# Performance work log

Measured on AMD Instinct MI355X. Metric: run time of the kernel, lower is better.

The kernel has to match this reference:

```python
import jax, jax.numpy as jnp
import numpy as np
import math

K = 3          # kernel_size
P_GEM = 3.0    # GeM power
EPS_GEM = 1e-6
EPS_NORM = 1e-12


def _l2n(x, axis):
    n = jnp.sqrt(jnp.sum(x * x, axis=axis, keepdims=True))
    return x / jnp.maximum(n, EPS_NORM)


def setup_inputs() -> dict:
    key = jax.random.key(0)
    ks = jax.random.split(key, 7)
    b, hw, c, nc = 32, 196, 768, 4096
    hidden = c  # mlp_ratio = 1
    return {
        "patch_tokens": jax.random.normal(ks[0], (b, hw, c), dtype=jnp.float32),
        "fc1_w": jax.random.normal(ks[1], (c, hidden), dtype=jnp.float32) * 0.02,
        "fc1_b": jnp.zeros((hidden,), dtype=jnp.float32),
        "fc2_w": jax.random.normal(ks[2], (hidden, c), dtype=jnp.float32) * 0.02,
        "fc2_b": jnp.zeros((c,), dtype=jnp.float32),
        "head_w": jax.random.normal(ks[3], (c, nc), dtype=jnp.float32) * 0.02,
        "head_b": jnp.zeros((nc,), dtype=jnp.float32),
    }


def reference(patch_tokens, fc1_w, fc1_b, fc2_w, fc2_b, head_w, head_b):
    b, hw, c = patch_tokens.shape
    h = w = int(math.sqrt(hw))

    # ---- SpaceSelfAware: pad -> unfold (3x3 local windows) -> multiply ----
    img = jnp.transpose(patch_tokens, (0, 2, 1)).reshape(b, c, h, w)
    # ZeroPad2d((left=1, right=1, top=2, bottom=0)) for kernel_size=3
    padded = jnp.pad(img, ((0, 0), (0, 0), (K - 1, 0), (K // 2, K // 2)))
    # stack the 9 shifted views, row-major over (ki, kj) matching nn.Unfold
    wins = jnp.stack(
        [padded[:, :, ki:ki + h, kj:kj + w] for ki in range(K) for kj in range(K)],
        axis=2,
    )  # (b, c, 9, h, w)
    y = wins.reshape(b, c, K, K, hw)
    y = jnp.transpose(y, (0, 4, 1, 2, 3))  # (b, hw, c, K, K)
    ssa = patch_tokens[:, :, :, None, None] * y  # (b, hw, c, K, K)

    # ---- space_fusion: L2Norm(dim=1) then GeM(p=3) over the KxK window ----
    ssa = _l2n(ssa, axis=1)
    pooled = jnp.mean(jnp.clip(ssa, EPS_GEM, None) ** P_GEM, axis=(-2, -1)) ** (1.0 / P_GEM)  # (b, hw, c)

    # ---- residual + L2 normalize over channels + Mlp ----
    tokens = pooled + patch_tokens
    tokens = _l2n(tokens, axis=-1)
    hdn = jax.nn.gelu(tokens @ fc1_w + fc1_b, approximate=False)
    tokens = hdn @ fc2_w + fc2_b  # (b, hw, c)

    # ---- GeMHead: GeM(p=3) over tokens, linear to nc, L2 normalize ----
    g = jnp.mean(jnp.clip(tokens, EPS_GEM, None) ** P_GEM, axis=1) ** (1.0 / P_GEM)  # (b, c)
    desc = g @ head_w + head_b  # (b, nc)
    desc = _l2n(desc, axis=-1)
    return desc
```

## Files before the change

### kernel.cpp

```cpp
#include <hip/hip_runtime.h>
#include <hip/hip_bf16.h>
#include <math.h>

#define B   32
#define P   196
#define C   768
#define NC  4096
#define HH  14
#define KSPLIT 24
#define NT  12
#define M6  6272
#define TW  (768 * 32)
#define TM  (M6 * 32)

typedef _Float16 half8 __attribute__((ext_vector_type(8)));
typedef _Float16 half4 __attribute__((ext_vector_type(4)));
typedef float f32x4 __attribute__((ext_vector_type(4)));

#define GLOAD_LDS16(g, l)                                                      \
    __builtin_amdgcn_global_load_lds(                                          \
        (const __attribute__((address_space(1))) void*)(g),                    \
        (__attribute__((address_space(3))) void*)(l), 16, 0, 0)

__global__ __launch_bounds__(256) void k_ssa(const float* __restrict__ t,
                                             float* __restrict__ pre) {
    const int b = blockIdx.y, c0 = blockIdx.x * 16;
    __shared__ float xp_[256 * 16];
    __shared__ float part[4][9][16];
    __shared__ float inv_norm[9][16];
    const int tid = threadIdx.x;
    const int cc = tid & 15, g = tid >> 4, wv = tid >> 6;

#pragma unroll
    for (int q = 0; q < 16; ++q) xp_[q * 256 + tid] = 0.0f;
    __syncthreads();

    for (int idx = tid; idx < 784; idx += 256) {
        const int p = idx >> 2, c = (idx & 3) * 4;
        const int i = p / HH, j = p % HH;
        *(float4*)&xp_[((i + 2) * 16 + (j + 1)) * 16 + c] =
            *(const float4*)&t[((size_t)b * P + p) * C + c0 + c];
    }
    __syncthreads();

    float s[9] = {};
    {
        int i = 0, j = g;
        if (j >= HH) { j -= HH; i = 1; }
        for (int p = g; p < P; p += 16) {
            const int base = ((i + 2) * 16 + (j + 1)) * 16 + cc;
            const float xp = xp_[base];
            const float xp2 = xp * xp;
#pragma unroll
            for (int k = 0; k < 9; ++k) {
                const int off = ((k / 3) - 2) * 16 + (k % 3) - 1;
                const float nb = xp_[base + off * 16];
                s[k] += xp2 * nb * nb;
            }
            j += 2; ++i;
            if (j >= HH) { j -= HH; ++i; }
        }
    }
#pragma unroll
    for (int k = 0; k < 9; ++k) {
        float r = s[k];
        r += __shfl_xor(r, 16);
        r += __shfl_xor(r, 32);
        s[k] = r;
    }
    if ((tid & 63) < 16) {
#pragma unroll
        for (int k = 0; k < 9; ++k) part[wv][k][cc] = s[k];
    }
    __syncthreads();
    if (tid < 144) {
        const int k = tid >> 4, c2 = tid & 15;
        const float t4 = part[0][k][c2] + part[1][k][c2] +
                         part[2][k][c2] + part[3][k][c2];
        inv_norm[k][c2] = 1.0f / fmaxf(sqrtf(t4), 1e-12f);
    }
    __syncthreads();

    float invn[9];
#pragma unroll
    for (int k = 0; k < 9; ++k) invn[k] = inv_norm[k][cc];

    {
        int i = 0, j = g;
        if (j >= HH) { j -= HH; i = 1; }
        for (int p = g; p < P; p += 16) {
            const int base = ((i + 2) * 16 + (j + 1)) * 16 + cc;
            const float xp = xp_[base];
            float acc = 0.0f;
#pragma unroll
            for (int k = 0; k < 9; ++k) {
                const int off = ((k / 3) - 2) * 16 + (k % 3) - 1;
                const float v = xp * xp_[base + off * 16];
                const float u = fmaxf(v * invn[k], 1e-6f);
                acc += u * u * u;
            }
            pre[((size_t)b * P + p) * C + c0 + cc] =
                cbrtf(acc * (1.0f / 9.0f)) + xp;
            j += 2; ++i;
            if (j >= HH) { j -= HH; ++i; }
        }
    }
}

__global__ __launch_bounds__(256) void k_rownorm(const float* __restrict__ in,
                                                 _Float16* __restrict__ outP) {
    const int row = blockIdx.x;
    const float* r = in + (size_t)row * C;
    const int tid = threadIdx.x;
    float vals[3];
    float s = 0.0f;
#pragma unroll
    for (int q = 0; q < 3; ++q) {
        vals[q] = r[tid + q * 256];
        s += vals[q] * vals[q];
    }
    __shared__ float partial[4];
    __shared__ float inv;
    __shared__ _Float16 nrm[C];
#pragma unroll
    for (int off = 32; off > 0; off >>= 1) s += __shfl_xor(s, off);
    if ((tid & 63) == 0) partial[tid >> 6] = s;
    __syncthreads();
    if (tid == 0)
        inv = 1.0f / fmaxf(sqrtf(partial[0] + partial[1] + partial[2] + partial[3]), 1e-12f);
    __syncthreads();
#pragma unroll
    for (int q = 0; q < 3; ++q)
        nrm[tid + q * 256] = (_Float16)(vals[q] * inv);
    __syncthreads();
    if (tid < 96) {
        const half8 v = *(const half8*)&nrm[tid * 8];
        const int kb = tid >> 2;
        const int slot = (tid & 3) ^ ((row >> 1) & 3);
        *(half8*)&outP[(size_t)kb * TM + (size_t)row * 32 + slot * 8] = v;
    }
}

__global__ __launch_bounds__(256) void k_wt(const float* __restrict__ W,
                                            _Float16* __restrict__ WtP) {
    __shared__ float tt[32][33];
    const int k0 = blockIdx.x * 32, n0 = blockIdx.y * 32;
    const int r = threadIdx.x / 32, c = threadIdx.x % 32;
#pragma unroll
    for (int q = 0; q < 4; ++q)
        tt[r + q * 8][c] = W[(size_t)(k0 + r + q * 8) * C + n0 + c];
    __syncthreads();
    const int nl = threadIdx.x >> 3, h = threadIdx.x & 7;
    const int n = n0 + nl;
    half4 v;
#pragma unroll
    for (int j = 0; j < 4; ++j) v[j] = (_Float16)tt[h * 4 + j][nl];
    const int el = (h * 4) ^ (((n >> 1) & 3) << 3);
    *(half4*)&WtP[(size_t)blockIdx.x * TW + (size_t)n * 32 + el] = v;
}

template <bool GELU>
__global__ __launch_bounds__(256) void k_mfma_gemm(
    const _Float16* __restrict__ TokP,
    const _Float16* __restrict__ WtP,
    const float* __restrict__ bias,
    _Float16* __restrict__ Cout) {
    __shared__ _Float16 lA[3][2][64][32];
    __shared__ _Float16 lB[3][2][64][32];
    const int tid = threadIdx.x;
    const int w = tid >> 6, l = tid & 63;
    const int l15 = l & 15, lk = l >> 4;

    const int lid = blockIdx.x;
    int vm, vn;
    if (lid < 1152) { vm = (lid / 96) * 8 + (lid & 7); vn = (lid % 96) >> 3; }
    else            { const int r = lid - 1152; vm = 96 + r / 12; vn = r % 12; }
    const int m0 = vm * 64, n0 = vn * 64;
    const int wn = (w & 1) * 32, wm = (w >> 1) * 32;

    f32x4 acc[2][2] = {};

    const int kbsel = w & 1;
    const bool isB = (w >= 2);
    const _Float16* srcBase =
        isB ? (TokP + (size_t)m0 * 32) : (WtP + (size_t)n0 * 32);
    const size_t tileStride = isB ? (size_t)TM : (size_t)TW;
    _Float16* dst0 = isB ? &lB[0][kbsel][0][0] : &lA[0][kbsel][0][0];

#define ISSUE(tt, bf_)                                                         \
    {   const _Float16* s_ = srcBase + (size_t)(2 * (tt) + kbsel) * tileStride;\
        _Float16* d_ = dst0 + (size_t)(bf_) * 4096;                            \
        GLOAD_LDS16(s_ + l * 8,        d_ + l * 8);                            \
        GLOAD_LDS16(s_ + 512 + l * 8,  d_ + 512 + l * 8);                      \
        GLOAD_LDS16(s_ + 1024 + l * 8, d_ + 1024 + l * 8);                     \
        GLOAD_LDS16(s_ + 1536 + l * 8, d_ + 1536 + l * 8); }

    ISSUE(0, 0); ISSUE(1, 1); ISSUE(2, 2);

    for (int t = 0; t < NT; ++t) {
        if (t < NT - 2)       asm volatile("s_waitcnt vmcnt(8)" ::: "memory");
        else if (t == NT - 2) asm volatile("s_waitcnt vmcnt(4)" ::: "memory");
        else                  asm volatile("s_waitcnt vmcnt(0)" ::: "memory");
        __builtin_amdgcn_s_barrier();
        __builtin_amdgcn_sched_barrier(0);

        const int buf = t % 3;
#pragma unroll
        for (int kk = 0; kk < 2; ++kk) {
            half8 af[2], bf[2];
#pragma unroll
            for (int fa = 0; fa < 2; ++fa) {
                const int rowA = wn + fa * 16 + l15;
                const int colA = (lk ^ ((rowA >> 1) & 3)) * 8;
                af[fa] = *(const half8*)&lA[buf][kk][rowA][colA];
            }
#pragma unroll
            for (int fb = 0; fb < 2; ++fb) {
                const int rowB = wm + fb * 16 + l15;
                const int colB = (lk ^ ((rowB >> 1) & 3)) * 8;
                bf[fb] = *(const half8*)&lB[buf][kk][rowB][colB];
            }
#pragma unroll
            for (int fa = 0; fa < 2; ++fa)
#pragma unroll
                for (int fb = 0; fb < 2; ++fb)
                    acc[fa][fb] = __builtin_amdgcn_mfma_f32_16x16x32_f16(
                        af[fa], bf[fb], acc[fa][fb], 0, 0, 0);
        }
        asm volatile("s_waitcnt lgkmcnt(0)" ::: "memory");
        __builtin_amdgcn_s_barrier();
        __builtin_amdgcn_sched_barrier(0);
        if (t < NT - 3) ISSUE(t + 3, buf);
    }
#undef ISSUE

#pragma unroll
    for (int fa = 0; fa < 2; ++fa) {
        const int nb = n0 + wn + fa * 16 + lk * 4;
        const float4 bv = *(const float4*)&bias[nb];
#pragma unroll
        for (int fb = 0; fb < 2; ++fb) {
            const int m = m0 + wm + fb * 16 + l15;
            half4 o;
            if (GELU) {
#pragma unroll
                for (int rr = 0; rr < 4; ++rr) {
                    float v = acc[fa][fb][rr] + ((const float*)&bv)[rr];
                    v = 0.5f * v * (1.0f + erff(v * 0.70710678118654752f));
                    o[rr] = (_Float16)v;
                }
                const int el = (nb & 31) ^ (((m >> 1) & 3) << 3);
                *(half4*)&Cout[(size_t)(nb >> 5) * TM + (size_t)m * 32 + el] = o;
            } else {
#pragma unroll
                for (int rr = 0; rr < 4; ++rr)
                    o[rr] = (_Float16)(acc[fa][fb][rr] + ((const float*)&bv)[rr]);
                *(half4*)&Cout[(size_t)m * C + nb] = o;
            }
        }
    }
}

__global__ __launch_bounds__(256) void k_gempool(const _Float16* __restrict__ tk,
                                                 float* __restrict__ g) {
    const int b = blockIdx.x / 12;
    const int c0 = (blockIdx.x % 12) * 64;
    const int tid = threadIdx.x;
    const int cc = tid & 63, pg = tid >> 6;
    float s = 0.0f;
    for (int p = pg * 49; p < pg * 49 + 49; ++p) {
        const float v = fmaxf((float)tk[((size_t)b * P + p) * C + c0 + cc], 1e-6f);
        s += v * v * v;
    }
    __shared__ float part[4][64];
    part[pg][cc] = s;
    __syncthreads();
    if (tid < 64) {
        const float t4 = part[0][cc] + part[1][cc] + part[2][cc] + part[3][cc];
        g[b * C + c0 + cc] = cbrtf(t4 * (1.0f / (float)P));
    }
}

__global__ __launch_bounds__(256) void k_head1(const float* __restrict__ g,
                                               const float* __restrict__ W,
                                               float* __restrict__ partial) {
    const int n0 = blockIdx.x * 64;
    const int k0 = blockIdx.y * 32;
    __shared__ float gs[32][32];
    __shared__ float part[4][32][64];
    const int tid = threadIdx.x;

    for (int idx = tid; idx < 32 * 32; idx += 256)
        gs[idx >> 5][idx & 31] = g[(idx >> 5) * C + k0 + (idx & 31)];
    __syncthreads();

    const int c = tid & 63, q = tid >> 6;
    float acc[32] = {};
#pragma unroll
    for (int kk = 0; kk < 8; ++kk) {
        const int k = q * 8 + kk;
        const float wv = W[(size_t)(k0 + k) * NC + n0 + c];
#pragma unroll
        for (int b = 0; b < 32; ++b) acc[b] += gs[b][k] * wv;
    }
#pragma unroll
    for (int b = 0; b < 32; ++b) part[q][b][c] = acc[b];
    __syncthreads();

    for (int o = tid; o < 32 * 64; o += 256) {
        const int b = o >> 6, cc = o & 63;
        const float v = part[0][b][cc] + part[1][b][cc] +
                        part[2][b][cc] + part[3][b][cc];
        partial[((size_t)blockIdx.y * 32 + b) * NC + n0 + cc] = v;
    }
}

__global__ __launch_bounds__(256) void k_head2(const float* __restrict__ partial,
                                               const float* __restrict__ hb,
                                               float* __restrict__ out) {
    const int n = blockIdx.x * 256 + threadIdx.x;
    const int b = blockIdx.y;
    float s = hb[n];
#pragma unroll
    for (int ks = 0; ks < KSPLIT; ++ks)
        s += partial[((size_t)ks * 32 + b) * NC + n];
    out[(size_t)b * NC + n] = s;
}

__global__ __launch_bounds__(256) void k_outnorm(float* __restrict__ out) {
    const int b = blockIdx.x;
    float* r = out + (size_t)b * NC;
    const int tid = threadIdx.x;
    float v[16];
    float s = 0.0f;
#pragma unroll
    for (int q = 0; q < 16; ++q) {
        v[q] = r[tid + q * 256];
        s += v[q] * v[q];
    }
    __shared__ float partial[4];
    __shared__ float inv;
#pragma unroll
    for (int off = 32; off > 0; off >>= 1) s += __shfl_xor(s, off);
    if ((tid & 63) == 0) partial[tid >> 6] = s;
    __syncthreads();
    if (tid == 0)
        inv = 1.0f / fmaxf(sqrtf(partial[0] + partial[1] + partial[2] + partial[3]), 1e-12f);
    __syncthreads();
#pragma unroll
    for (int q = 0; q < 16; ++q) r[tid + q * 256] = v[q] * inv;
}

extern "C" void kernel_launch(void* const* d_in, const int* in_sizes, int n_in,
                              void* d_out, int out_size, void* d_ws, size_t ws_size,
                              hipStream_t stream) {
    const float* patch  = (const float*)d_in[0];
    const float* fc1_w  = (const float*)d_in[1];
    const float* fc1_b  = (const float*)d_in[2];
    const float* fc2_w  = (const float*)d_in[3];
    const float* fc2_b  = (const float*)d_in[4];
    const float* head_w = (const float*)d_in[5];
    const float* head_b = (const float*)d_in[6];
    float* out = (float*)d_out;

    const size_t big = (size_t)B * P * C;
    float*    pre  = (float*)d_ws;
    _Float16* tokP = (_Float16*)(pre + big);
    _Float16* hdnP = tokP + big;
    _Float16* wt1  = hdnP + big;
    _Float16* wt2  = wt1 + C * C;
    float*    gbuf = (float*)(wt2 + C * C);
    float*    hpart = gbuf + B * C;
    _Float16* tok2 = (_Float16*)pre;

    k_ssa<<<dim3(C / 16, B), dim3(256), 0, stream>>>(patch, pre);
    k_wt<<<dim3(C / 32, C / 32), dim3(256), 0, stream>>>(fc1_w, wt1);
    k_wt<<<dim3(C / 32, C / 32), dim3(256), 0, stream>>>(fc2_w, wt2);
    k_rownorm<<<dim3(B * P), dim3(256), 0, stream>>>(pre, tokP);
    k_mfma_gemm<true><<<dim3(1176), dim3(256), 0, stream>>>(
        tokP, wt1, fc1_b, hdnP);
    k_mfma_gemm<false><<<dim3(1176), dim3(256), 0, stream>>>(
        hdnP, wt2, fc2_b, tok2);
    k_gempool<<<dim3(B * 12), dim3(256), 0, stream>>>(tok2, gbuf);
    k_head1<<<dim3(NC / 64, KSPLIT), dim3(256), 0, stream>>>(gbuf, head_w, hpart);
    k_head2<<<dim3(NC / 256, B), dim3(256), 0, stream>>>(hpart, head_b, out);
    k_outnorm<<<dim3(B), dim3(256), 0, stream>>>(out);
}
```

Baseline: 94.03 us.

## Fold row normalization into fc1 epilogue and emit packed fp16 from SSA

The SSA kernel now writes unnormalized fp16 tokens directly in the swizzled GEMM layout, together with per-channel-block partial sums of squares. A small kernel reduces these partials into per-row inverse norms, and the fc1 GEMM epilogue multiplies the accumulator by that inverse norm. This removes the fp32 intermediate write/read and the separate row-norm kernel, and the two weight transposes are merged into one launch. The trade-off is that fp16 rounding now happens before normalization rather than after, and there is an extra partial-sum buffer and reduction kernel.

```diff
diff --git a/kernel.cpp b/kernel.cpp
--- a/kernel.cpp
+++ b/kernel.cpp
@@ -23,11 +23,13 @@
         (__attribute__((address_space(3))) void*)(l), 16, 0, 0)
 
 __global__ __launch_bounds__(256) void k_ssa(const float* __restrict__ t,
-                                             float* __restrict__ pre) {
-    const int b = blockIdx.y, c0 = blockIdx.x * 16;
+                                             _Float16* __restrict__ outP,
+                                             float* __restrict__ partial) {
+    const int b = blockIdx.y, cb = blockIdx.x, c0 = cb * 16;
     __shared__ float xp_[256 * 16];
     __shared__ float part[4][9][16];
     __shared__ float inv_norm[9][16];
+    __shared__ _Float16 outT[P][16];
     const int tid = threadIdx.x;
     const int cc = tid & 15, g = tid >> 4, wv = tid >> 6;
 
@@ -99,50 +101,46 @@
                 const float u = fmaxf(v * invn[k], 1e-6f);
                 acc += u * u * u;
             }
-            pre[((size_t)b * P + p) * C + c0 + cc] =
-                cbrtf(acc * (1.0f / 9.0f)) + xp;
+            const float val = cbrtf(acc * (1.0f / 9.0f)) + xp;
+            float rs = val * val;
+            rs += __shfl_xor(rs, 1);
+            rs += __shfl_xor(rs, 2);
+            rs += __shfl_xor(rs, 4);
+            rs += __shfl_xor(rs, 8);
+            outT[p][cc] = (_Float16)val;
+            if (cc == 0) partial[(size_t)cb * M6 + b * P + p] = rs;
             j += 2; ++i;
             if (j >= HH) { j -= HH; ++i; }
         }
     }
-}
-
-__global__ __launch_bounds__(256) void k_rownorm(const float* __restrict__ in,
-                                                 _Float16* __restrict__ outP) {
-    const int row = blockIdx.x;
-    const float* r = in + (size_t)row * C;
-    const int tid = threadIdx.x;
-    float vals[3];
-    float s = 0.0f;
-#pragma unroll
-    for (int q = 0; q < 3; ++q) {
-        vals[q] = r[tid + q * 256];
-        s += vals[q] * vals[q];
-    }
-    __shared__ float partial[4];
-    __shared__ float inv;
-    __shared__ _Float16 nrm[C];
-#pragma unroll
-    for (int off = 32; off > 0; off >>= 1) s += __shfl_xor(s, off);
-    if ((tid & 63) == 0) partial[tid >> 6] = s;
-    __syncthreads();
-    if (tid == 0)
-        inv = 1.0f / fmaxf(sqrtf(partial[0] + partial[1] + partial[2] + partial[3]), 1e-12f);
-    __syncthreads();
-#pragma unroll
-    for (int q = 0; q < 3; ++q)
-        nrm[tid + q * 256] = (_Float16)(vals[q] * inv);
-    __syncthreads();
-    if (tid < 96) {
-        const half8 v = *(const half8*)&nrm[tid * 8];
-        const int kb = tid >> 2;
-        const int slot = (tid & 3) ^ ((row >> 1) & 3);
+    __syncthreads();
+    const int kb = cb >> 1, kbase = (cb & 1) * 16;
+    for (int idx = tid; idx < P * 2; idx += 256) {
+        const int p = idx >> 1, h = idx & 1;
+        const half8 v = *(const half8*)&outT[p][h * 8];
+        const int row = b * P + p;
+        const int slot = ((kbase + h * 8) >> 3) ^ ((row >> 1) & 3);
         *(half8*)&outP[(size_t)kb * TM + (size_t)row * 32 + slot * 8] = v;
     }
 }
 
-__global__ __launch_bounds__(256) void k_wt(const float* __restrict__ W,
-                                            _Float16* __restrict__ WtP) {
+__global__ __launch_bounds__(256) void k_inv(const float* __restrict__ partial,
+                                             float* __restrict__ inv) {
+    const int row = blockIdx.x * 256 + threadIdx.x;
+    if (row < M6) {
+        float s = 0.0f;
+#pragma unroll 8
+        for (int cb = 0; cb < 48; ++cb) s += partial[(size_t)cb * M6 + row];
+        inv[row] = 1.0f / fmaxf(sqrtf(s), 1e-12f);
+    }
+}
+
+__global__ __launch_bounds__(256) void k_wt(const float* __restrict__ W1,
+                                            const float* __restrict__ W2,
+                                            _Float16* __restrict__ O1,
+                                            _Float16* __restrict__ O2) {
+    const float* W = blockIdx.z ? W2 : W1;
+    _Float16* WtP = blockIdx.z ? O2 : O1;
     __shared__ float tt[32][33];
     const int k0 = blockIdx.x * 32, n0 = blockIdx.y * 32;
     const int r = threadIdx.x / 32, c = threadIdx.x % 32;
@@ -164,6 +162,7 @@
     const _Float16* __restrict__ TokP,
     const _Float16* __restrict__ WtP,
     const float* __restrict__ bias,
+    const float* __restrict__ invv,
     _Float16* __restrict__ Cout) {
     __shared__ _Float16 lA[3][2][64][32];
     __shared__ _Float16 lB[3][2][64][32];
@@ -234,6 +233,12 @@
     }
 #undef ISSUE
 
+    float invm[2];
+    if (GELU) {
+#pragma unroll
+        for (int fb = 0; fb < 2; ++fb)
+            invm[fb] = invv[m0 + wm + fb * 16 + l15];
+    }
 #pragma unroll
     for (int fa = 0; fa < 2; ++fa) {
         const int nb = n0 + wn + fa * 16 + lk * 4;
@@ -245,7 +250,7 @@
             if (GELU) {
 #pragma unroll
                 for (int rr = 0; rr < 4; ++rr) {
-                    float v = acc[fa][fb][rr] + ((const float*)&bv)[rr];
+                    float v = acc[fa][fb][rr] * invm[fb] + ((const float*)&bv)[rr];
                     v = 0.5f * v * (1.0f + erff(v * 0.70710678118654752f));
                     o[rr] = (_Float16)v;
                 }
@@ -364,23 +369,24 @@
     float* out = (float*)d_out;
 
     const size_t big = (size_t)B * P * C;
-    float*    pre  = (float*)d_ws;
-    _Float16* tokP = (_Float16*)(pre + big);
-    _Float16* hdnP = tokP + big;
-    _Float16* wt1  = hdnP + big;
-    _Float16* wt2  = wt1 + C * C;
-    float*    gbuf = (float*)(wt2 + C * C);
+    _Float16* tokU  = (_Float16*)d_ws;
+    _Float16* hdnP  = tokU + big;
+    _Float16* wt1   = hdnP + big;
+    _Float16* wt2   = wt1 + C * C;
+    float*    spart = (float*)(wt2 + C * C);
+    float*    invv  = spart + 48 * (size_t)M6;
+    float*    gbuf  = invv + M6;
     float*    hpart = gbuf + B * C;
-    _Float16* tok2 = (_Float16*)pre;
-
-    k_ssa<<<dim3(C / 16, B), dim3(256), 0, stream>>>(patch, pre);
-    k_wt<<<dim3(C / 32, C / 32), dim3(256), 0, stream>>>(fc1_w, wt1);
-    k_wt<<<dim3(C / 32, C / 32), dim3(256), 0, stream>>>(fc2_w, wt2);
-    k_rownorm<<<dim3(B * P), dim3(256), 0, stream>>>(pre, tokP);
+    _Float16* tok2  = (_Float16*)(hpart + (size_t)KSPLIT * 32 * NC);
+
+    k_ssa<<<dim3(48, B), dim3(256), 0, stream>>>(patch, tokU, spart);
+    k_inv<<<dim3((M6 + 255) / 256), dim3(256), 0, stream>>>(spart, invv);
+    k_wt<<<dim3(C / 32, C / 32, 2), dim3(256), 0, stream>>>(
+        fc1_w, fc2_w, wt1, wt2);
     k_mfma_gemm<true><<<dim3(1176), dim3(256), 0, stream>>>(
-        tokP, wt1, fc1_b, hdnP);
+        tokU, wt1, fc1_b, invv, hdnP);
     k_mfma_gemm<false><<<dim3(1176), dim3(256), 0, stream>>>(
-        hdnP, wt2, fc2_b, tok2);
+        hdnP, wt2, fc2_b, nullptr, tok2);
     k_gempool<<<dim3(B * 12), dim3(256), 0, stream>>>(tok2, gbuf);
     k_head1<<<dim3(NC / 64, KSPLIT), dim3(256), 0, stream>>>(gbuf, head_w, hpart);
     k_head2<<<dim3(NC / 256, B), dim3(256), 0, stream>>>(hpart, head_b, out);
```

Measured after the change: 93.31 us. No clear change (-0.8%).
